# Kernel optimization log

Measured on AMD Instinct MI355X. Metric: run time of the kernel, lower is better.

Reference implementation:

```python
import jax, jax.numpy as jnp
import numpy as np

N_NODES = 50000
N_EDGES = 800000
D = 128
LEAKY_SLOPE = 0.01
EPS = 1e-12


def _sage_conv(x, edge_index, W_l, b_l, W_r):
    # PyG SAGEConv (aggr='mean', root_weight=True, normalize=True):
    #   out = lin_l(mean_{j in N(i)} x_j) + lin_r(x_i); out = out / ||out||_2
    src = edge_index[0]
    dst = edge_index[1]
    # gather source features, scatter-mean onto destinations  [N, D]
    summed = jax.ops.segment_sum(x[src], dst, num_segments=N_NODES)
    cnt = jax.ops.segment_sum(jnp.ones((src.shape[0],), x.dtype), dst,
                              num_segments=N_NODES)
    mean = summed / jnp.maximum(cnt, 1.0)[:, None]
    out = mean @ W_l.T + b_l + x @ W_r.T
    norm = jnp.linalg.norm(out, axis=-1, keepdims=True)
    return out / jnp.maximum(norm, EPS)


def setup_inputs() -> dict:
    key = jax.random.key(0)
    ks = jax.random.split(key, 8)
    scale = 1.0 / np.sqrt(D)
    x = jax.random.normal(ks[0], (N_NODES, D), dtype=jnp.float32)
    edge_index = jax.random.randint(ks[1], (2, N_EDGES), 0, N_NODES, dtype=jnp.int64)
    return {
        "x": x,
        "edge_index": edge_index,
        "W1_l": jax.random.normal(ks[2], (D, D), dtype=jnp.float32) * scale,
        "b1_l": jax.random.normal(ks[3], (D,), dtype=jnp.float32) * scale,
        "W1_r": jax.random.normal(ks[4], (D, D), dtype=jnp.float32) * scale,
        "W2_l": jax.random.normal(ks[5], (D, D), dtype=jnp.float32) * scale,
        "b2_l": jax.random.normal(ks[6], (D,), dtype=jnp.float32) * scale,
        "W2_r": jax.random.normal(ks[7], (D, D), dtype=jnp.float32) * scale,
    }


def reference(x, edge_index, W1_l, b1_l, W1_r, W2_l, b2_l, W2_r):
    h1 = jax.nn.leaky_relu(_sage_conv(x, edge_index, W1_l, b1_l, W1_r),
                           negative_slope=LEAKY_SLOPE)
    h2 = _sage_conv(h1, edge_index, W2_l, b2_l, W2_r)
    return h1 + h2
```

## Files before the change

kernel.cpp:

```cpp
#include <hip/hip_runtime.h>

#define N_NODES 50000
#define N_EDGES 800000
#define D 128
#define NBKT 196
#define BKT_CAP 5120

typedef __attribute__((ext_vector_type(8))) short bf16x8;
typedef __attribute__((ext_vector_type(4))) float f32x4;

__device__ __forceinline__ float bf2f(unsigned short u) {
    unsigned int x = ((unsigned int)u) << 16;
    return __builtin_bit_cast(float, x);
}
__device__ __forceinline__ unsigned short f2bf(float f) {
    unsigned int u = __builtin_bit_cast(unsigned int, f);
    unsigned int r = (u + 0x7fffu + ((u >> 16) & 1u)) >> 16;
    return (unsigned short)r;
}


__global__ __launch_bounds__(256) void k_part(const int* __restrict__ ei,
                                              int* __restrict__ bcnt,
                                              uint* __restrict__ bucket) {
    __shared__ int hist[NBKT];
    __shared__ int base[NBKT];
    int tid = threadIdx.x;
    for (int i = tid; i < NBKT; i += 256) hist[i] = 0;
    __syncthreads();
    int e0 = blockIdx.x * 2048;
    uint meta[8];
    #pragma unroll
    for (int i = 0; i < 8; ++i) {
        int e = e0 + i * 256 + tid;
        uint m = 0xFFFFFFFFu;
        if (e < N_EDGES) {
            int dst = ei[N_EDGES + e];
            int b = dst >> 8;
            int dl = dst & 255;
            int r = atomicAdd(&hist[b], 1);
            m = ((uint)b << 21) | ((uint)dl << 13) | (uint)r;
        }
        meta[i] = m;
    }
    __syncthreads();
    for (int i = tid; i < NBKT; i += 256)
        base[i] = hist[i] ? atomicAdd(&bcnt[i], hist[i]) : 0;
    __syncthreads();
    #pragma unroll
    for (int i = 0; i < 8; ++i) {
        int e = e0 + i * 256 + tid;
        if (e < N_EDGES) {
            uint m = meta[i];
            int b = (int)(m >> 21);
            int dl = (int)((m >> 13) & 255);
            int r = (int)(m & 8191);
            int src = ei[e];
            int pos = base[b] + r;
            if (pos < BKT_CAP)
                bucket[(size_t)b * BKT_CAP + pos] = ((uint)dl << 16) | (uint)src;
        }
    }
}

__global__ __launch_bounds__(256) void k_hist(const int* __restrict__ bcnt,
                                              const uint* __restrict__ bucket,
                                              int* __restrict__ deg) {
    __shared__ int hist[256];
    int b = blockIdx.x, tid = threadIdx.x;
    hist[tid] = 0;
    __syncthreads();
    int n = bcnt[b]; if (n > BKT_CAP) n = BKT_CAP;
    for (int i = tid; i < n; i += 256)
        atomicAdd(&hist[(bucket[(size_t)b * BKT_CAP + i] >> 16) & 255], 1);
    __syncthreads();
    int node = b * 256 + tid;
    if (node < N_NODES) deg[node] = hist[tid];
}

__global__ __launch_bounds__(256) void k_scan1(const int* __restrict__ deg,
                                               int* __restrict__ rowp,
                                               int* __restrict__ bsum) {
    __shared__ int s[256];
    int t = threadIdx.x;
    int i = blockIdx.x * 256 + t;
    int v = (i < N_NODES) ? deg[i] : 0;
    s[t] = v;
    __syncthreads();
    for (int off = 1; off < 256; off <<= 1) {
        int u = (t >= off) ? s[t - off] : 0;
        __syncthreads();
        s[t] += u;
        __syncthreads();
    }
    if (i < N_NODES) rowp[i] = s[t] - v;
    if (t == 255) bsum[blockIdx.x] = s[255];
}

__global__ __launch_bounds__(256) void k_scan2(int* __restrict__ bsum, int nb) {
    __shared__ int s[256];
    int t = threadIdx.x;
    int v = (t < nb) ? bsum[t] : 0;
    s[t] = v;
    __syncthreads();
    for (int off = 1; off < 256; off <<= 1) {
        int u = (t >= off) ? s[t - off] : 0;
        __syncthreads();
        s[t] += u;
        __syncthreads();
    }
    if (t < nb) bsum[t] = s[t] - v;
}

__global__ __launch_bounds__(256) void k_scan3(int* __restrict__ rowp,
                                               const int* __restrict__ bsum) {
    int i = blockIdx.x * 256 + threadIdx.x;
    if (i < N_NODES) rowp[i] += bsum[blockIdx.x];
    if (i == 0) rowp[N_NODES] = N_EDGES;
}

__global__ __launch_bounds__(256) void k_sort(const int* __restrict__ bcnt,
                                              const uint* __restrict__ bucket,
                                              const int* __restrict__ rowp,
                                              int* __restrict__ colx) {
    __shared__ int fil[256];
    __shared__ int rp[256];
    int b = blockIdx.x, tid = threadIdx.x;
    fil[tid] = 0;
    int node = b * 256 + tid;
    rp[tid] = (node < N_NODES) ? rowp[node] : 0;
    __syncthreads();
    int n = bcnt[b]; if (n > BKT_CAP) n = BKT_CAP;
    for (int i = tid; i < n; i += 256) {
        uint w = bucket[(size_t)b * BKT_CAP + i];
        int dl = (int)((w >> 16) & 255);
        int src = (int)(w & 0xFFFF);
        int p = rp[dl] + atomicAdd(&fil[dl], 1);
        colx[p] = src;
    }
}


__global__ __launch_bounds__(256) void k_cvt(const float* __restrict__ in,
                                             ushort* __restrict__ outb,
                                             uint* __restrict__ outq, int n4) {
    int i = blockIdx.x * 256 + threadIdx.x;
    if (i >= n4) return;
    float4 v = ((const float4*)in)[i];
    ushort4 o;
    o.x = f2bf(v.x); o.y = f2bf(v.y); o.z = f2bf(v.z); o.w = f2bf(v.w);
    ((ushort4*)outb)[i] = o;
    int q = __builtin_amdgcn_cvt_pk_fp8_f32(v.x, v.y, 0, false);
    q = __builtin_amdgcn_cvt_pk_fp8_f32(v.z, v.w, q, true);
    outq[i] = (uint)q;
}

__global__ __launch_bounds__(256) void k_cvtw(const float* __restrict__ w0,
                                              const float* __restrict__ w1,
                                              const float* __restrict__ w2,
                                              const float* __restrict__ w3,
                                              ushort* o0, ushort* o1,
                                              ushort* o2, ushort* o3) {
    int b = blockIdx.x >> 4;
    int i = (blockIdx.x & 15) * 256 + threadIdx.x;
    const float* in = (b == 0) ? w0 : (b == 1) ? w1 : (b == 2) ? w2 : w3;
    ushort*     out = (b == 0) ? o0 : (b == 1) ? o1 : (b == 2) ? o2 : o3;
    float4 v = ((const float4*)in)[i];
    ushort4 o;
    o.x = f2bf(v.x); o.y = f2bf(v.y); o.z = f2bf(v.z); o.w = f2bf(v.w);
    ((ushort4*)out)[i] = o;
}

__global__ __launch_bounds__(256) void k_cvt8(const ushort* __restrict__ inb,
                                              uint* __restrict__ outq, int n8) {
    int i = blockIdx.x * 256 + threadIdx.x;
    if (i >= n8) return;
    bf16x8 v = ((const bf16x8*)inb)[i];
    float f0 = bf2f((unsigned short)v[0]), f1 = bf2f((unsigned short)v[1]);
    float f2 = bf2f((unsigned short)v[2]), f3 = bf2f((unsigned short)v[3]);
    float f4 = bf2f((unsigned short)v[4]), f5 = bf2f((unsigned short)v[5]);
    float f6 = bf2f((unsigned short)v[6]), f7 = bf2f((unsigned short)v[7]);
    int q0 = __builtin_amdgcn_cvt_pk_fp8_f32(f0, f1, 0, false);
    q0 = __builtin_amdgcn_cvt_pk_fp8_f32(f2, f3, q0, true);
    int q1 = __builtin_amdgcn_cvt_pk_fp8_f32(f4, f5, 0, false);
    q1 = __builtin_amdgcn_cvt_pk_fp8_f32(f6, f7, q1, true);
    uint2 o; o.x = (uint)q0; o.y = (uint)q1;
    ((uint2*)outq)[i] = o;
}


__device__ __forceinline__ void acc4(float* a, unsigned int word) {
    a[0] += __builtin_amdgcn_cvt_f32_fp8(word, 0);
    a[1] += __builtin_amdgcn_cvt_f32_fp8(word, 1);
    a[2] += __builtin_amdgcn_cvt_f32_fp8(word, 2);
    a[3] += __builtin_amdgcn_cvt_f32_fp8(word, 3);
}
__device__ __forceinline__ void acc16(float* a, uint4 v) {
    acc4(a + 0, v.x); acc4(a + 4, v.y); acc4(a + 8, v.z); acc4(a + 12, v.w);
}

__global__ __launch_bounds__(256) void k_agg(const uint* __restrict__ Xq,
                                             const int* __restrict__ rowp,
                                             const int* __restrict__ colx,
                                             ushort* __restrict__ Mb) {
    int t = blockIdx.x * 256 + threadIdx.x;
    int node = t >> 4;
    int sl = threadIdx.x & 7;
    int half = (threadIdx.x >> 3) & 1;
    if (node >= N_NODES) return;
    int beg = rowp[node], end = rowp[node + 1];
    float a[16];
    #pragma unroll
    for (int q = 0; q < 16; ++q) a[q] = 0.f;
    int j = beg + half;
    for (; j + 6 < end; j += 8) {
        int s0 = colx[j], s1 = colx[j + 2], s2 = colx[j + 4], s3 = colx[j + 6];
        uint4 w0 = *(const uint4*)(Xq + (size_t)s0 * 32 + sl * 4);
        uint4 w1 = *(const uint4*)(Xq + (size_t)s1 * 32 + sl * 4);
        uint4 w2 = *(const uint4*)(Xq + (size_t)s2 * 32 + sl * 4);
        uint4 w3 = *(const uint4*)(Xq + (size_t)s3 * 32 + sl * 4);
        acc16(a, w0); acc16(a, w1); acc16(a, w2); acc16(a, w3);
    }
    for (; j < end; j += 2) {
        int s0 = colx[j];
        uint4 w0 = *(const uint4*)(Xq + (size_t)s0 * 32 + sl * 4);
        acc16(a, w0);
    }
    #pragma unroll
    for (int q = 0; q < 16; ++q) a[q] += __shfl_xor(a[q], 8, 64);
    if (half == 0) {
        float inv = 1.0f / fmaxf((float)(end - beg), 1.0f);
        bf16x8 o0, o1;
        #pragma unroll
        for (int q = 0; q < 8; ++q) o0[q] = (short)f2bf(a[q] * inv);
        #pragma unroll
        for (int q = 0; q < 8; ++q) o1[q] = (short)f2bf(a[q + 8] * inv);
        *(bf16x8*)(Mb + (size_t)node * D + sl * 16) = o0;
        *(bf16x8*)(Mb + (size_t)node * D + sl * 16 + 8) = o1;
    }
}


__global__ __launch_bounds__(256) void k_gemm(const ushort* __restrict__ Ab_m,
                                              const ushort* __restrict__ Ab_x,
                                              const ushort* __restrict__ Wl,
                                              const ushort* __restrict__ Wr,
                                              const float* __restrict__ bias,
                                              const ushort* __restrict__ h1b_in,
                                              float* __restrict__ out,
                                              ushort* __restrict__ h1b_out,
                                              int mode) {
    __shared__ ushort Wlds[32768];
    int tid = threadIdx.x;

    #pragma unroll
    for (int jj = 0; jj < 16; ++jj) {
        int n = jj * 256 + tid;
        int row = n >> 5, c16 = n & 31;
        const ushort* src = (c16 < 16) ? (Wl + row * 128 + c16 * 8)
                                       : (Wr + row * 128 + (c16 - 16) * 8);
        bf16x8 v = *(const bf16x8*)src;
        int slot = row * 32 + (c16 ^ (row & 7));
        *(bf16x8*)(Wlds + slot * 8) = v;
    }
    __syncthreads();

    int lane = tid & 63;
    int wid = tid >> 6;
    int r = lane & 15, g = lane >> 4;
    int row0 = blockIdx.x * 64 + wid * 16;
    int anode = row0 + r;
    bool avalid = anode < N_NODES;
    const ushort* am = Ab_m + (size_t)anode * D + g * 8;
    const ushort* ax = Ab_x + (size_t)anode * D + g * 8;

    f32x4 acc[8];
    #pragma unroll
    for (int c = 0; c < 8; ++c) acc[c] = (f32x4){0.f, 0.f, 0.f, 0.f};

    #pragma unroll
    for (int s = 0; s < 8; ++s) {
        bf16x8 a = (bf16x8){0, 0, 0, 0, 0, 0, 0, 0};
        if (avalid) a = *(const bf16x8*)((s < 4 ? am : ax) + (s & 3) * 32);
        #pragma unroll
        for (int c = 0; c < 8; ++c) {
            int wrow = c * 16 + r;
            int byte = (wrow * 512 + s * 64 + g * 16) ^ ((wrow & 7) << 4);
            bf16x8 b = *(const bf16x8*)((const char*)Wlds + byte);
            acc[c] = __builtin_amdgcn_mfma_f32_16x16x32_bf16(a, b, acc[c], 0, 0, 0);
        }
    }

    #pragma unroll
    for (int c = 0; c < 8; ++c) {
        float bv = bias[c * 16 + r];
        #pragma unroll
        for (int i = 0; i < 4; ++i) acc[c][i] += bv;
    }

    float ss[4];
    #pragma unroll
    for (int i = 0; i < 4; ++i) {
        float s = 0.f;
        #pragma unroll
        for (int c = 0; c < 8; ++c) s += acc[c][i] * acc[c][i];
        ss[i] = s;
    }
    #pragma unroll
    for (int m = 1; m < 16; m <<= 1) {
        #pragma unroll
        for (int i = 0; i < 4; ++i) ss[i] += __shfl_xor(ss[i], m, 64);
    }
    float rn[4];
    #pragma unroll
    for (int i = 0; i < 4; ++i) rn[i] = 1.0f / fmaxf(sqrtf(ss[i]), 1e-12f);

    #pragma unroll
    for (int i = 0; i < 4; ++i) {
        int row = row0 + 4 * g + i;
        if (row >= N_NODES) continue;
        #pragma unroll
        for (int c = 0; c < 8; ++c) {
            int col = c * 16 + r;
            float v = acc[c][i] * rn[i];
            if (mode == 0) {
                v = (v > 0.f) ? v : 0.01f * v;
                h1b_out[(size_t)row * D + col] = f2bf(v);
            } else {
                v += bf2f(h1b_in[(size_t)row * D + col]);
                out[(size_t)row * D + col] = v;
            }
        }
    }
}


extern "C" void kernel_launch(void* const* d_in, const int* in_sizes, int n_in,
                              void* d_out, int out_size, void* d_ws, size_t ws_size,
                              hipStream_t stream) {
    const float* x   = (const float*)d_in[0];
    const int*   ei  = (const int*)d_in[1];
    const float* W1l = (const float*)d_in[2];
    const float* b1l = (const float*)d_in[3];
    const float* W1r = (const float*)d_in[4];
    const float* W2l = (const float*)d_in[5];
    const float* b2l = (const float*)d_in[6];
    const float* W2r = (const float*)d_in[7];
    float* out = (float*)d_out;
    char*  ws  = (char*)d_ws;

    int*    bcnt = (int*)(ws + 0);
    int*    deg  = (int*)(ws + 1024);
    int*    rowp = (int*)(ws + 204800);
    int*    colx = (int*)(ws + 409600);
    ushort* xb   = (ushort*)(ws + 3609600);
    ushort* Mb   = (ushort*)(ws + 16409600);
    ushort* Wb   = (ushort*)(ws + 29209600);
    ushort* W1lb = Wb;
    ushort* W1rb = Wb + 16384;
    ushort* W2lb = Wb + 32768;
    ushort* W2rb = Wb + 49152;
    int*    bsum = (int*)(ws + 29340672);
    uint*   Q    = (uint*)(ws + 29341696);
    uint*   bkt  = (uint*)(ws + 35742208);

    hipMemsetAsync(bcnt, 0, 1024, stream);

    k_cvt <<<6250, 256, 0, stream>>>(x, xb, Q, (N_NODES * D) / 4);
    k_cvtw<<<64, 256, 0, stream>>>(W1l, W1r, W2l, W2r, W1lb, W1rb, W2lb, W2rb);

    const int NB = (N_NODES + 255) / 256;
    k_part<<<(N_EDGES + 2047) / 2048, 256, 0, stream>>>(ei, bcnt, bkt);
    k_hist<<<NBKT, 256, 0, stream>>>(bcnt, bkt, deg);
    k_scan1<<<NB, 256, 0, stream>>>(deg, rowp, bsum);
    k_scan2<<<1, 256, 0, stream>>>(bsum, NB);
    k_scan3<<<NB, 256, 0, stream>>>(rowp, bsum);
    k_sort<<<NBKT, 256, 0, stream>>>(bcnt, bkt, rowp, colx);

    const int NA = (N_NODES * 16 + 255) / 256;
    k_agg <<<NA, 256, 0, stream>>>(Q, rowp, colx, Mb);
    k_gemm<<<(N_NODES + 63) / 64, 256, 0, stream>>>(Mb, xb, W1lb, W1rb, b1l,
                                                    nullptr, out, xb, 0);
    k_cvt8<<<(N_NODES * D / 8 + 255) / 256, 256, 0, stream>>>(xb, Q, N_NODES * D / 8);
    k_agg <<<NA, 256, 0, stream>>>(Q, rowp, colx, Mb);
    k_gemm<<<(N_NODES + 63) / 64, 256, 0, stream>>>(Mb, xb, W2lb, W2rb, b2l,
                                                    xb, out, nullptr, 1);
}
```

Before: 213.9 us.

## Split neighbor aggregation into two feature-half passes with nontemporal stores

```diff
diff --git a/kernel.cpp b/kernel.cpp
--- a/kernel.cpp
+++ b/kernel.cpp
@@ -8,6 +8,7 @@
 
 typedef __attribute__((ext_vector_type(8))) short bf16x8;
 typedef __attribute__((ext_vector_type(4))) float f32x4;
+typedef __attribute__((ext_vector_type(4))) uint uint4v;
 
 __device__ __forceinline__ float bf2f(unsigned short u) {
     unsigned int x = ((unsigned int)u) << 16;
@@ -199,35 +200,37 @@
     acc4(a + 0, v.x); acc4(a + 4, v.y); acc4(a + 8, v.z); acc4(a + 12, v.w);
 }
 
-__global__ __launch_bounds__(256) void k_agg(const uint* __restrict__ Xq,
-                                             const int* __restrict__ rowp,
-                                             const int* __restrict__ colx,
-                                             ushort* __restrict__ Mb) {
+__global__ __launch_bounds__(256) void k_aggh(const uint* __restrict__ Xq,
+                                              const int* __restrict__ rowp,
+                                              const int* __restrict__ colx,
+                                              ushort* __restrict__ Mb,
+                                              int phase) {
     int t = blockIdx.x * 256 + threadIdx.x;
-    int node = t >> 4;
-    int sl = threadIdx.x & 7;
-    int half = (threadIdx.x >> 3) & 1;
+    int node = t >> 3;
+    int sl = threadIdx.x & 3;
+    int half = (threadIdx.x >> 2) & 1;
     if (node >= N_NODES) return;
     int beg = rowp[node], end = rowp[node + 1];
+    const uint* base = Xq + phase * 16 + sl * 4;
     float a[16];
     #pragma unroll
     for (int q = 0; q < 16; ++q) a[q] = 0.f;
     int j = beg + half;
     for (; j + 6 < end; j += 8) {
         int s0 = colx[j], s1 = colx[j + 2], s2 = colx[j + 4], s3 = colx[j + 6];
-        uint4 w0 = *(const uint4*)(Xq + (size_t)s0 * 32 + sl * 4);
-        uint4 w1 = *(const uint4*)(Xq + (size_t)s1 * 32 + sl * 4);
-        uint4 w2 = *(const uint4*)(Xq + (size_t)s2 * 32 + sl * 4);
-        uint4 w3 = *(const uint4*)(Xq + (size_t)s3 * 32 + sl * 4);
+        uint4 w0 = *(const uint4*)(base + (size_t)s0 * 32);
+        uint4 w1 = *(const uint4*)(base + (size_t)s1 * 32);
+        uint4 w2 = *(const uint4*)(base + (size_t)s2 * 32);
+        uint4 w3 = *(const uint4*)(base + (size_t)s3 * 32);
         acc16(a, w0); acc16(a, w1); acc16(a, w2); acc16(a, w3);
     }
     for (; j < end; j += 2) {
         int s0 = colx[j];
-        uint4 w0 = *(const uint4*)(Xq + (size_t)s0 * 32 + sl * 4);
+        uint4 w0 = *(const uint4*)(base + (size_t)s0 * 32);
         acc16(a, w0);
     }
     #pragma unroll
-    for (int q = 0; q < 16; ++q) a[q] += __shfl_xor(a[q], 8, 64);
+    for (int q = 0; q < 16; ++q) a[q] += __shfl_xor(a[q], 4, 64);
     if (half == 0) {
         float inv = 1.0f / fmaxf((float)(end - beg), 1.0f);
         bf16x8 o0, o1;
@@ -235,8 +238,9 @@
         for (int q = 0; q < 8; ++q) o0[q] = (short)f2bf(a[q] * inv);
         #pragma unroll
         for (int q = 0; q < 8; ++q) o1[q] = (short)f2bf(a[q + 8] * inv);
-        *(bf16x8*)(Mb + (size_t)node * D + sl * 16) = o0;
-        *(bf16x8*)(Mb + (size_t)node * D + sl * 16 + 8) = o1;
+        ushort* dst = Mb + (size_t)node * D + phase * 64 + sl * 16;
+        __builtin_nontemporal_store(__builtin_bit_cast(uint4v, o0), (uint4v*)dst);
+        __builtin_nontemporal_store(__builtin_bit_cast(uint4v, o1), (uint4v*)(dst + 8));
     }
 }
 
@@ -377,12 +381,14 @@
     k_scan3<<<NB, 256, 0, stream>>>(rowp, bsum);
     k_sort<<<NBKT, 256, 0, stream>>>(bcnt, bkt, rowp, colx);
 
-    const int NA = (N_NODES * 16 + 255) / 256;
-    k_agg <<<NA, 256, 0, stream>>>(Q, rowp, colx, Mb);
+    const int NH = (N_NODES * 8 + 255) / 256;
+    k_aggh<<<NH, 256, 0, stream>>>(Q, rowp, colx, Mb, 0);
+    k_aggh<<<NH, 256, 0, stream>>>(Q, rowp, colx, Mb, 1);
     k_gemm<<<(N_NODES + 63) / 64, 256, 0, stream>>>(Mb, xb, W1lb, W1rb, b1l,
                                                     nullptr, out, xb, 0);
     k_cvt8<<<(N_NODES * D / 8 + 255) / 256, 256, 0, stream>>>(xb, Q, N_NODES * D / 8);
-    k_agg <<<NA, 256, 0, stream>>>(Q, rowp, colx, Mb);
+    k_aggh<<<NH, 256, 0, stream>>>(Q, rowp, colx, Mb, 0);
+    k_aggh<<<NH, 256, 0, stream>>>(Q, rowp, colx, Mb, 1);
     k_gemm<<<(N_NODES + 63) / 64, 256, 0, stream>>>(Mb, xb, W2lb, W2rb, b2l,
                                                     xb, out, nullptr, 1);
 }
```

New measurement: 238.3 us. +11.4%, slower.

## Fuse conversion kernels, histogram with scan, and fp8 quantization into GEMM epilogue

Applied to the files above, without the earlier changes.

```diff
diff --git a/kernel.cpp b/kernel.cpp
--- a/kernel.cpp
+++ b/kernel.cpp
@@ -63,10 +63,12 @@
     }
 }
 
-__global__ __launch_bounds__(256) void k_hist(const int* __restrict__ bcnt,
-                                              const uint* __restrict__ bucket,
-                                              int* __restrict__ deg) {
+__global__ __launch_bounds__(256) void k_histscan(const int* __restrict__ bcnt,
+                                                  const uint* __restrict__ bucket,
+                                                  int* __restrict__ rowp,
+                                                  int* __restrict__ bsum) {
     __shared__ int hist[256];
+    __shared__ int s[256];
     int b = blockIdx.x, tid = threadIdx.x;
     hist[tid] = 0;
     __syncthreads();
@@ -74,27 +76,18 @@
     for (int i = tid; i < n; i += 256)
         atomicAdd(&hist[(bucket[(size_t)b * BKT_CAP + i] >> 16) & 255], 1);
     __syncthreads();
+    int v = hist[tid];
+    s[tid] = v;
+    __syncthreads();
+    for (int off = 1; off < 256; off <<= 1) {
+        int u = (tid >= off) ? s[tid - off] : 0;
+        __syncthreads();
+        s[tid] += u;
+        __syncthreads();
+    }
     int node = b * 256 + tid;
-    if (node < N_NODES) deg[node] = hist[tid];
-}
-
-__global__ __launch_bounds__(256) void k_scan1(const int* __restrict__ deg,
-                                               int* __restrict__ rowp,
-                                               int* __restrict__ bsum) {
-    __shared__ int s[256];
-    int t = threadIdx.x;
-    int i = blockIdx.x * 256 + t;
-    int v = (i < N_NODES) ? deg[i] : 0;
-    s[t] = v;
-    __syncthreads();
-    for (int off = 1; off < 256; off <<= 1) {
-        int u = (t >= off) ? s[t - off] : 0;
-        __syncthreads();
-        s[t] += u;
-        __syncthreads();
-    }
-    if (i < N_NODES) rowp[i] = s[t] - v;
-    if (t == 255) bsum[blockIdx.x] = s[255];
+    if (node < N_NODES) rowp[node] = s[tid] - v;
+    if (tid == 255) bsum[b] = s[255];
 }
 
 __global__ __launch_bounds__(256) void k_scan2(int* __restrict__ bsum, int nb) {
@@ -141,51 +134,41 @@
 }
 
 
-__global__ __launch_bounds__(256) void k_cvt(const float* __restrict__ in,
-                                             ushort* __restrict__ outb,
-                                             uint* __restrict__ outq, int n4) {
-    int i = blockIdx.x * 256 + threadIdx.x;
-    if (i >= n4) return;
-    float4 v = ((const float4*)in)[i];
-    ushort4 o;
-    o.x = f2bf(v.x); o.y = f2bf(v.y); o.z = f2bf(v.z); o.w = f2bf(v.w);
-    ((ushort4*)outb)[i] = o;
-    int q = __builtin_amdgcn_cvt_pk_fp8_f32(v.x, v.y, 0, false);
-    q = __builtin_amdgcn_cvt_pk_fp8_f32(v.z, v.w, q, true);
-    outq[i] = (uint)q;
-}
-
-__global__ __launch_bounds__(256) void k_cvtw(const float* __restrict__ w0,
-                                              const float* __restrict__ w1,
-                                              const float* __restrict__ w2,
-                                              const float* __restrict__ w3,
-                                              ushort* o0, ushort* o1,
-                                              ushort* o2, ushort* o3) {
-    int b = blockIdx.x >> 4;
-    int i = (blockIdx.x & 15) * 256 + threadIdx.x;
-    const float* in = (b == 0) ? w0 : (b == 1) ? w1 : (b == 2) ? w2 : w3;
-    ushort*     out = (b == 0) ? o0 : (b == 1) ? o1 : (b == 2) ? o2 : o3;
-    float4 v = ((const float4*)in)[i];
-    ushort4 o;
-    o.x = f2bf(v.x); o.y = f2bf(v.y); o.z = f2bf(v.z); o.w = f2bf(v.w);
-    ((ushort4*)out)[i] = o;
-}
-
-__global__ __launch_bounds__(256) void k_cvt8(const ushort* __restrict__ inb,
-                                              uint* __restrict__ outq, int n8) {
-    int i = blockIdx.x * 256 + threadIdx.x;
-    if (i >= n8) return;
-    bf16x8 v = ((const bf16x8*)inb)[i];
-    float f0 = bf2f((unsigned short)v[0]), f1 = bf2f((unsigned short)v[1]);
-    float f2 = bf2f((unsigned short)v[2]), f3 = bf2f((unsigned short)v[3]);
-    float f4 = bf2f((unsigned short)v[4]), f5 = bf2f((unsigned short)v[5]);
-    float f6 = bf2f((unsigned short)v[6]), f7 = bf2f((unsigned short)v[7]);
-    int q0 = __builtin_amdgcn_cvt_pk_fp8_f32(f0, f1, 0, false);
-    q0 = __builtin_amdgcn_cvt_pk_fp8_f32(f2, f3, q0, true);
-    int q1 = __builtin_amdgcn_cvt_pk_fp8_f32(f4, f5, 0, false);
-    q1 = __builtin_amdgcn_cvt_pk_fp8_f32(f6, f7, q1, true);
-    uint2 o; o.x = (uint)q0; o.y = (uint)q1;
-    ((uint2*)outq)[i] = o;
+__global__ __launch_bounds__(256) void k_cvtall(const float* __restrict__ x,
+                                                ushort* __restrict__ xb,
+                                                uint* __restrict__ xq,
+                                                const float* __restrict__ w0,
+                                                const float* __restrict__ w1,
+                                                const float* __restrict__ w2,
+                                                const float* __restrict__ w3,
+                                                ushort* o0, ushort* o1,
+                                                ushort* o2, ushort* o3,
+                                                int* __restrict__ bcnt) {
+    int blk = blockIdx.x;
+    int tid = threadIdx.x;
+    if (blk < 6250) {
+        int i = blk * 256 + tid;
+        if (i >= (N_NODES * D) / 4) return;
+        float4 v = ((const float4*)x)[i];
+        ushort4 o;
+        o.x = f2bf(v.x); o.y = f2bf(v.y); o.z = f2bf(v.z); o.w = f2bf(v.w);
+        ((ushort4*)xb)[i] = o;
+        int q = __builtin_amdgcn_cvt_pk_fp8_f32(v.x, v.y, 0, false);
+        q = __builtin_amdgcn_cvt_pk_fp8_f32(v.z, v.w, q, true);
+        xq[i] = (uint)q;
+    } else if (blk < 6314) {
+        int wb = blk - 6250;
+        int b = wb >> 4;
+        int i = (wb & 15) * 256 + tid;
+        const float* in = (b == 0) ? w0 : (b == 1) ? w1 : (b == 2) ? w2 : w3;
+        ushort*     out = (b == 0) ? o0 : (b == 1) ? o1 : (b == 2) ? o2 : o3;
+        float4 v = ((const float4*)in)[i];
+        ushort4 o;
+        o.x = f2bf(v.x); o.y = f2bf(v.y); o.z = f2bf(v.z); o.w = f2bf(v.w);
+        ((ushort4*)out)[i] = o;
+    } else {
+        bcnt[tid] = 0;
+    }
 }
 
 
@@ -249,6 +232,7 @@
                                               const ushort* __restrict__ h1b_in,
                                               float* __restrict__ out,
                                               ushort* __restrict__ h1b_out,
+                                              unsigned char* __restrict__ q_out,
                                               int mode) {
     __shared__ ushort Wlds[32768];
     int tid = threadIdx.x;
@@ -326,6 +310,8 @@
             if (mode == 0) {
                 v = (v > 0.f) ? v : 0.01f * v;
                 h1b_out[(size_t)row * D + col] = f2bf(v);
+                int qb = __builtin_amdgcn_cvt_pk_fp8_f32(v, v, 0, false);
+                q_out[(size_t)row * D + col] = (unsigned char)(qb & 0xFF);
             } else {
                 v += bf2f(h1b_in[(size_t)row * D + col]);
                 out[(size_t)row * D + col] = v;
@@ -350,7 +336,6 @@
     char*  ws  = (char*)d_ws;
 
     int*    bcnt = (int*)(ws + 0);
-    int*    deg  = (int*)(ws + 1024);
     int*    rowp = (int*)(ws + 204800);
     int*    colx = (int*)(ws + 409600);
     ushort* xb   = (ushort*)(ws + 3609600);
@@ -364,15 +349,12 @@
     uint*   Q    = (uint*)(ws + 29341696);
     uint*   bkt  = (uint*)(ws + 35742208);
 
-    hipMemsetAsync(bcnt, 0, 1024, stream);
-
-    k_cvt <<<6250, 256, 0, stream>>>(x, xb, Q, (N_NODES * D) / 4);
-    k_cvtw<<<64, 256, 0, stream>>>(W1l, W1r, W2l, W2r, W1lb, W1rb, W2lb, W2rb);
+    k_cvtall<<<6315, 256, 0, stream>>>(x, xb, Q, W1l, W1r, W2l, W2r,
+                                       W1lb, W1rb, W2lb, W2rb, bcnt);
 
     const int NB = (N_NODES + 255) / 256;
     k_part<<<(N_EDGES + 2047) / 2048, 256, 0, stream>>>(ei, bcnt, bkt);
-    k_hist<<<NBKT, 256, 0, stream>>>(bcnt, bkt, deg);
-    k_scan1<<<NB, 256, 0, stream>>>(deg, rowp, bsum);
+    k_histscan<<<NBKT, 256, 0, stream>>>(bcnt, bkt, rowp, bsum);
     k_scan2<<<1, 256, 0, stream>>>(bsum, NB);
     k_scan3<<<NB, 256, 0, stream>>>(rowp, bsum);
     k_sort<<<NBKT, 256, 0, stream>>>(bcnt, bkt, rowp, colx);
@@ -380,9 +362,10 @@
     const int NA = (N_NODES * 16 + 255) / 256;
     k_agg <<<NA, 256, 0, stream>>>(Q, rowp, colx, Mb);
     k_gemm<<<(N_NODES + 63) / 64, 256, 0, stream>>>(Mb, xb, W1lb, W1rb, b1l,
-                                                    nullptr, out, xb, 0);
-    k_cvt8<<<(N_NODES * D / 8 + 255) / 256, 256, 0, stream>>>(xb, Q, N_NODES * D / 8);
+                                                    nullptr, out, xb,
+                                                    (unsigned char*)Q, 0);
     k_agg <<<NA, 256, 0, stream>>>(Q, rowp, colx, Mb);
     k_gemm<<<(N_NODES + 63) / 64, 256, 0, stream>>>(Mb, xb, W2lb, W2rb, b2l,
-                                                    xb, out, nullptr, 1);
-}
+                                                    xb, out, nullptr,
+                                                    nullptr, 1);
+}
```

After: 205.4 us. 4.0% less time.
